# Kernel tuning notes

Hardware: AMD Instinct MI355X
Metric: run time of the kernel (lower is better)

Reference implementation:

```python
import jax, jax.numpy as jnp
import numpy as np

TOP_K = 32

def setup_inputs() -> dict:
    key = jax.random.key(0)
    x = jax.random.normal(key, (4096, 32768), dtype=jnp.float32)
    return {"x": x}

def reference(x) -> jnp.ndarray:
    bsz, d_sae = x.shape
    k = min(TOP_K, d_sae)
    # top-k indices per row (unsorted order does not matter for masking)
    _, idxs = jax.lax.top_k(x, k)  # [batch, k]
    rows = jnp.arange(bsz)[:, None]  # [batch, 1]
    mask = jnp.zeros_like(x).at[rows, idxs].set(1.0)
    return mask * x
```

## Files before the change

kernel.cpp:

```cpp
#include <hip/hip_runtime.h>

#define TOPK    32
#define ROW     32768
#define THREADS 512
#define WAVES   8
#define VPT     16
#define BINS    2048
#define CAP     2048

__device__ __forceinline__ unsigned int f2key(float f) {
    unsigned int u = __float_as_uint(f);
    return u ^ (0x80000000u | (unsigned int)((int)u >> 31));
}
__device__ __forceinline__ float key2f(unsigned int k) {
    unsigned int u = (k & 0x80000000u) ? (k & 0x7fffffffu) : ~k;
    return __uint_as_float(u);
}

struct Shared {
    unsigned int hist[BINS];
    unsigned int wsum[WAVES];
    unsigned int sel_g, sel_gabove;
    unsigned int sel_bin, sel_above;
    unsigned int cand_cnt;
    unsigned int cnt_s;
    float        Tf;
    unsigned int idxcut;
    float        cf[CAP];
    unsigned int cidx[CAP];
};

__device__ __forceinline__ void hist_select(Shared& sh, int t, int lane,
                                            int wave, unsigned int kk) {
    const int base = wave * 256 + lane * 4;
    unsigned int h0 = sh.hist[base + 0], h1 = sh.hist[base + 1];
    unsigned int h2 = sh.hist[base + 2], h3 = sh.hist[base + 3];
    unsigned int p = h0 + h1 + h2 + h3;
    unsigned int s = p;
#pragma unroll
    for (int off = 1; off < 64; off <<= 1) {
        unsigned int vv = __shfl_down(s, off);
        if (lane + off < 64) s += vv;
    }
    if (lane == 0) sh.wsum[wave] = s;
    __syncthreads();

    if (t == 0) {
        unsigned int above = 0; int g = WAVES - 1;
        for (int w = WAVES - 1; w >= 0; --w) {
            if (above + sh.wsum[w] >= kk) { g = w; break; }
            above += sh.wsum[w];
        }
        sh.sel_g = (unsigned int)g; sh.sel_gabove = above;
    }
    __syncthreads();

    if (wave == (int)sh.sel_g) {
        unsigned int a = sh.sel_gabove + (s - p);
        unsigned int hh[4] = {h0, h1, h2, h3};
#pragma unroll
        for (int j = 3; j >= 0; --j) {
            unsigned int h = hh[j];
            if (a < kk && a + h >= kk) {
                sh.sel_bin = (unsigned int)(base + j);
                sh.sel_above = a;
            }
            a += h;
        }
    }
    __syncthreads();
}

__global__ __launch_bounds__(THREADS, 4) void topk_mask_kernel(
    const float* __restrict__ x, float* __restrict__ out) {

    __shared__ Shared sh;
    const int row  = blockIdx.x;
    const int t    = threadIdx.x;
    const int lane = t & 63;
    const int wave = t >> 6;

    const float4* __restrict__ xin =
        reinterpret_cast<const float4*>(x + (size_t)row * ROW);
    float4* __restrict__ xout =
        reinterpret_cast<float4*>(out + (size_t)row * ROW);

    float4 v[VPT];
#pragma unroll
    for (int i = 0; i < VPT; ++i) v[i] = xin[i * THREADS + t];

#pragma unroll
    for (int b = 0; b < 4; ++b) sh.hist[t + b * THREADS] = 0;
    if (t == 0) sh.cand_cnt = 0;
    __syncthreads();

    float m = -__builtin_inff();
#pragma unroll
    for (int i = 0; i < VPT; ++i)
        m = fmaxf(m, fmaxf(fmaxf(v[i].x, v[i].y), fmaxf(v[i].z, v[i].w)));

    atomicAdd(&sh.hist[f2key(m) >> 21], 1u);
    __syncthreads();

    hist_select(sh, t, lane, wave, TOPK);

    const float L = key2f(sh.sel_bin << 21);

#pragma unroll
    for (int i = 0; i < VPT; ++i) {
#pragma unroll
        for (int j = 0; j < 4; ++j) {
            float f = (&v[i].x)[j];
            if (f >= L) {
                unsigned int pos = atomicAdd(&sh.cand_cnt, 1u);
                if (pos < CAP) {
                    sh.cf[pos]   = f;
                    sh.cidx[pos] = (unsigned int)((i * THREADS + t) * 4 + j);
                }
            }
        }
    }
    __syncthreads();
    const unsigned int C = sh.cand_cnt;

    if (C <= CAP) {
        for (unsigned int i = t; i < C; i += THREADS) {
            float ki = sh.cf[i]; unsigned int ii = sh.cidx[i];
            unsigned int r = 0;
            for (unsigned int j = 0; j < C; ++j) {
                float kj = sh.cf[j];
                unsigned int ij = sh.cidx[j];
                r += (kj > ki || (kj == ki && ij < ii)) ? 1u : 0u;
            }
            if (r == TOPK - 1) { sh.Tf = ki; sh.idxcut = ii; }
        }
        __syncthreads();
        const float T = sh.Tf;
        const unsigned int ic = sh.idxcut;
#pragma unroll
        for (int i = 0; i < VPT; ++i) {
            float4 o;
#pragma unroll
            for (int j = 0; j < 4; ++j) {
                float f = (&v[i].x)[j];
                unsigned int idx = (unsigned int)((i * THREADS + t) * 4 + j);
                (&o.x)[j] = (f > T || (f == T && idx <= ic)) ? f : 0.0f;
            }
            xout[i * THREADS + t] = o;
        }
        return;
    }

    unsigned int prefix = 0; int pbits = 0;
    unsigned int kk = TOPK, e = 0;
    for (int r = 0; r < 3; ++r) {
        const int shift = (r == 0) ? 21 : (r == 1 ? 10 : 0);
        const int bits  = (r == 2) ? 10 : 11;
        const unsigned int msk = (1u << bits) - 1u;
        __syncthreads();
#pragma unroll
        for (int b = 0; b < 4; ++b) sh.hist[t + b * THREADS] = 0;
        __syncthreads();
#pragma unroll
        for (int i = 0; i < VPT; ++i) {
#pragma unroll
            for (int j = 0; j < 4; ++j) {
                unsigned int key = f2key((&v[i].x)[j]);
                bool match = (pbits == 0) || ((key >> (32 - pbits)) == prefix);
                if (match) atomicAdd(&sh.hist[(key >> shift) & msk], 1u);
            }
        }
        __syncthreads();
        hist_select(sh, t, lane, wave, kk);
        kk = kk - sh.sel_above;
        e  = sh.hist[sh.sel_bin];
        prefix = (prefix << bits) | sh.sel_bin;
        pbits += bits;
    }
    const unsigned int T = prefix;

    unsigned int Cc = ROW;
    if (e != kk) {
        unsigned int lo = 0, hi = ROW;
        while (hi - lo > 1u) {
            unsigned int mid = (lo + hi) >> 1;
            __syncthreads();
            if (t == 0) sh.cnt_s = 0;
            __syncthreads();
            unsigned int c = 0;
#pragma unroll
            for (int i = 0; i < VPT; ++i) {
#pragma unroll
                for (int j = 0; j < 4; ++j) {
                    unsigned int key = f2key((&v[i].x)[j]);
                    unsigned int idx = (unsigned int)((i * THREADS + t) * 4 + j);
                    if (key == T && idx < mid) ++c;
                }
            }
            if (c) atomicAdd(&sh.cnt_s, c);
            __syncthreads();
            if (sh.cnt_s >= kk) hi = mid; else lo = mid;
        }
        Cc = hi;
    }

#pragma unroll
    for (int i = 0; i < VPT; ++i) {
        float4 o;
#pragma unroll
        for (int j = 0; j < 4; ++j) {
            float f = (&v[i].x)[j];
            unsigned int key = f2key(f);
            unsigned int idx = (unsigned int)((i * THREADS + t) * 4 + j);
            (&o.x)[j] = (key > T || (key == T && idx < Cc)) ? f : 0.0f;
        }
        xout[i * THREADS + t] = o;
    }
}

extern "C" void kernel_launch(void* const* d_in, const int* in_sizes, int n_in,
                              void* d_out, int out_size, void* d_ws, size_t ws_size,
                              hipStream_t stream) {
    const float* x = (const float*)d_in[0];
    float* out = (float*)d_out;
    const int rows = in_sizes[0] / ROW;
    topk_mask_kernel<<<rows, THREADS, 0, stream>>>(x, out);
}
```

Measured before the change: 217.1 us.

## Zero output with memset and scatter only top-k values from kernel

Drops the full masked write of every row in favour of a hipMemsetAsync that zeroes the output, after which the kernel scatters only the selected top-k elements. It also removes the shared-memory threshold broadcast and one block barrier in the candidate path. The memset still writes the whole output, so total write traffic stays roughly the same but moves into a separate fill pass. If the timer counts both launches, the extra launch and the memset bandwidth may cancel the gain.

```diff
diff --git a/kernel.cpp b/kernel.cpp
--- a/kernel.cpp
+++ b/kernel.cpp
@@ -24,8 +24,6 @@
     unsigned int sel_bin, sel_above;
     unsigned int cand_cnt;
     unsigned int cnt_s;
-    float        Tf;
-    unsigned int idxcut;
     float        cf[CAP];
     unsigned int cidx[CAP];
 };
@@ -71,7 +69,7 @@
     __syncthreads();
 }
 
-__global__ __launch_bounds__(THREADS, 4) void topk_mask_kernel(
+__global__ __launch_bounds__(THREADS, 4) void topk_scatter_kernel(
     const float* __restrict__ x, float* __restrict__ out) {
 
     __shared__ Shared sh;
@@ -82,8 +80,7 @@
 
     const float4* __restrict__ xin =
         reinterpret_cast<const float4*>(x + (size_t)row * ROW);
-    float4* __restrict__ xout =
-        reinterpret_cast<float4*>(out + (size_t)row * ROW);
+    float* __restrict__ orow = out + (size_t)row * ROW;
 
     float4 v[VPT];
 #pragma unroll
@@ -132,21 +129,7 @@
                 unsigned int ij = sh.cidx[j];
                 r += (kj > ki || (kj == ki && ij < ii)) ? 1u : 0u;
             }
-            if (r == TOPK - 1) { sh.Tf = ki; sh.idxcut = ii; }
-        }
-        __syncthreads();
-        const float T = sh.Tf;
-        const unsigned int ic = sh.idxcut;
-#pragma unroll
-        for (int i = 0; i < VPT; ++i) {
-            float4 o;
-#pragma unroll
-            for (int j = 0; j < 4; ++j) {
-                float f = (&v[i].x)[j];
-                unsigned int idx = (unsigned int)((i * THREADS + t) * 4 + j);
-                (&o.x)[j] = (f > T || (f == T && idx <= ic)) ? f : 0.0f;
-            }
-            xout[i * THREADS + t] = o;
+            if (r < TOPK) orow[ii] = ki;
         }
         return;
     }
@@ -206,15 +189,13 @@
 
 #pragma unroll
     for (int i = 0; i < VPT; ++i) {
-        float4 o;
 #pragma unroll
         for (int j = 0; j < 4; ++j) {
             float f = (&v[i].x)[j];
             unsigned int key = f2key(f);
             unsigned int idx = (unsigned int)((i * THREADS + t) * 4 + j);
-            (&o.x)[j] = (key > T || (key == T && idx < Cc)) ? f : 0.0f;
-        }
-        xout[i * THREADS + t] = o;
+            if (key > T || (key == T && idx < Cc)) orow[idx] = f;
+        }
     }
 }
 
@@ -224,5 +205,6 @@
     const float* x = (const float*)d_in[0];
     float* out = (float*)d_out;
     const int rows = in_sizes[0] / ROW;
-    topk_mask_kernel<<<rows, THREADS, 0, stream>>>(x, out);
-}
+    hipMemsetAsync(out, 0, (size_t)out_size * sizeof(float), stream);
+    topk_scatter_kernel<<<rows, THREADS, 0, stream>>>(x, out);
+}
```

Result: slower. 239.4 us (+10.2%).

## Make blocks persistent and double-buffer row loads in registers across rows

Applied to the files above, without the earlier changes.

Launches 256 persistent blocks that each handle a contiguous run of rows. Each block prefetches the next row into a second register buffer while it processes the current one, so global load latency overlaps the histogram and selection work. Barriers are replaced with an LDS-only waitcnt plus s_barrier, which avoids waiting on outstanding global loads. The cost is doubled register use (occupancy hint lowered to 2 blocks), reliance on rows dividing evenly by 256, and only 256 blocks, which may leave compute units idle.

```diff
diff --git a/kernel.cpp b/kernel.cpp
--- a/kernel.cpp
+++ b/kernel.cpp
@@ -7,6 +7,7 @@
 #define VPT     16
 #define BINS    2048
 #define CAP     2048
+#define BLOCKS  256
 
 __device__ __forceinline__ unsigned int f2key(float f) {
     unsigned int u = __float_as_uint(f);
@@ -15,6 +16,11 @@
 __device__ __forceinline__ float key2f(unsigned int k) {
     unsigned int u = (k & 0x80000000u) ? (k & 0x7fffffffu) : ~k;
     return __uint_as_float(u);
+}
+
+__device__ __forceinline__ void bar_lds() {
+    asm volatile("s_waitcnt lgkmcnt(0)" ::: "memory");
+    __builtin_amdgcn_s_barrier();
 }
 
 struct Shared {
@@ -43,7 +49,7 @@
         if (lane + off < 64) s += vv;
     }
     if (lane == 0) sh.wsum[wave] = s;
-    __syncthreads();
+    bar_lds();
 
     if (t == 0) {
         unsigned int above = 0; int g = WAVES - 1;
@@ -53,7 +59,7 @@
         }
         sh.sel_g = (unsigned int)g; sh.sel_gabove = above;
     }
-    __syncthreads();
+    bar_lds();
 
     if (wave == (int)sh.sel_g) {
         unsigned int a = sh.sel_gabove + (s - p);
@@ -68,39 +74,24 @@
             a += h;
         }
     }
-    __syncthreads();
-}
-
-__global__ __launch_bounds__(THREADS, 4) void topk_mask_kernel(
-    const float* __restrict__ x, float* __restrict__ out) {
-
-    __shared__ Shared sh;
-    const int row  = blockIdx.x;
-    const int t    = threadIdx.x;
-    const int lane = t & 63;
-    const int wave = t >> 6;
-
-    const float4* __restrict__ xin =
-        reinterpret_cast<const float4*>(x + (size_t)row * ROW);
-    float4* __restrict__ xout =
-        reinterpret_cast<float4*>(out + (size_t)row * ROW);
-
-    float4 v[VPT];
-#pragma unroll
-    for (int i = 0; i < VPT; ++i) v[i] = xin[i * THREADS + t];
-
+    bar_lds();
+}
+
+__device__ __forceinline__ void process_row(Shared& sh, const float4 (&v)[VPT],
+                                            float* __restrict__ orow,
+                                            int t, int lane, int wave) {
 #pragma unroll
     for (int b = 0; b < 4; ++b) sh.hist[t + b * THREADS] = 0;
     if (t == 0) sh.cand_cnt = 0;
-    __syncthreads();
 
     float m = -__builtin_inff();
 #pragma unroll
     for (int i = 0; i < VPT; ++i)
         m = fmaxf(m, fmaxf(fmaxf(v[i].x, v[i].y), fmaxf(v[i].z, v[i].w)));
 
+    bar_lds();
     atomicAdd(&sh.hist[f2key(m) >> 21], 1u);
-    __syncthreads();
+    bar_lds();
 
     hist_select(sh, t, lane, wave, TOPK);
 
@@ -120,7 +111,7 @@
             }
         }
     }
-    __syncthreads();
+    bar_lds();
     const unsigned int C = sh.cand_cnt;
 
     if (C <= CAP) {
@@ -134,9 +125,10 @@
             }
             if (r == TOPK - 1) { sh.Tf = ki; sh.idxcut = ii; }
         }
-        __syncthreads();
+        bar_lds();
         const float T = sh.Tf;
         const unsigned int ic = sh.idxcut;
+        float4* __restrict__ xout = reinterpret_cast<float4*>(orow);
 #pragma unroll
         for (int i = 0; i < VPT; ++i) {
             float4 o;
@@ -157,10 +149,10 @@
         const int shift = (r == 0) ? 21 : (r == 1 ? 10 : 0);
         const int bits  = (r == 2) ? 10 : 11;
         const unsigned int msk = (1u << bits) - 1u;
-        __syncthreads();
+        bar_lds();
 #pragma unroll
         for (int b = 0; b < 4; ++b) sh.hist[t + b * THREADS] = 0;
-        __syncthreads();
+        bar_lds();
 #pragma unroll
         for (int i = 0; i < VPT; ++i) {
 #pragma unroll
@@ -170,7 +162,7 @@
                 if (match) atomicAdd(&sh.hist[(key >> shift) & msk], 1u);
             }
         }
-        __syncthreads();
+        bar_lds();
         hist_select(sh, t, lane, wave, kk);
         kk = kk - sh.sel_above;
         e  = sh.hist[sh.sel_bin];
@@ -184,9 +176,9 @@
         unsigned int lo = 0, hi = ROW;
         while (hi - lo > 1u) {
             unsigned int mid = (lo + hi) >> 1;
-            __syncthreads();
+            bar_lds();
             if (t == 0) sh.cnt_s = 0;
-            __syncthreads();
+            bar_lds();
             unsigned int c = 0;
 #pragma unroll
             for (int i = 0; i < VPT; ++i) {
@@ -198,12 +190,13 @@
                 }
             }
             if (c) atomicAdd(&sh.cnt_s, c);
-            __syncthreads();
+            bar_lds();
             if (sh.cnt_s >= kk) hi = mid; else lo = mid;
         }
         Cc = hi;
     }
 
+    float4* __restrict__ xout = reinterpret_cast<float4*>(orow);
 #pragma unroll
     for (int i = 0; i < VPT; ++i) {
         float4 o;
@@ -215,6 +208,47 @@
             (&o.x)[j] = (key > T || (key == T && idx < Cc)) ? f : 0.0f;
         }
         xout[i * THREADS + t] = o;
+    }
+}
+
+__global__ __launch_bounds__(THREADS, 2) void topk_pipelined_kernel(
+    const float* __restrict__ x, float* __restrict__ out, int rpb) {
+
+    __shared__ Shared sh;
+    const int t    = threadIdx.x;
+    const int lane = t & 63;
+    const int wave = t >> 6;
+    const int row0 = blockIdx.x * rpb;
+
+    float4 vA[VPT], vB[VPT];
+
+    {
+        const float4* __restrict__ xin =
+            reinterpret_cast<const float4*>(x + (size_t)row0 * ROW);
+#pragma unroll
+        for (int i = 0; i < VPT; ++i) vA[i] = xin[i * THREADS + t];
+    }
+
+    for (int r = 0; r < rpb; r += 2) {
+        if (r + 1 < rpb) {
+            const float4* __restrict__ xin =
+                reinterpret_cast<const float4*>(x + (size_t)(row0 + r + 1) * ROW);
+#pragma unroll
+            for (int i = 0; i < VPT; ++i) vB[i] = xin[i * THREADS + t];
+        }
+        __builtin_amdgcn_sched_barrier(0);
+        process_row(sh, vA, out + (size_t)(row0 + r) * ROW, t, lane, wave);
+
+        if (r + 1 < rpb) {
+            if (r + 2 < rpb) {
+                const float4* __restrict__ xin =
+                    reinterpret_cast<const float4*>(x + (size_t)(row0 + r + 2) * ROW);
+#pragma unroll
+                for (int i = 0; i < VPT; ++i) vA[i] = xin[i * THREADS + t];
+            }
+            __builtin_amdgcn_sched_barrier(0);
+            process_row(sh, vB, out + (size_t)(row0 + r + 1) * ROW, t, lane, wave);
+        }
     }
 }
 
@@ -224,5 +258,6 @@
     const float* x = (const float*)d_in[0];
     float* out = (float*)d_out;
     const int rows = in_sizes[0] / ROW;
-    topk_mask_kernel<<<rows, THREADS, 0, stream>>>(x, out);
-}
+    const int rpb  = rows / BLOCKS;
+    topk_pipelined_kernel<<<BLOCKS, THREADS, 0, stream>>>(x, out, rpb);
+}
```

Result: slower. 676.0 us (+211.3%).
